# Kernel optimization log

Hardware: AMD Instinct MI355X
Metric: run time of the kernel (lower is better)

The kernel has to match this reference:

```python
import jax, jax.numpy as jnp
import numpy as np

PATCH = 32      # patch_size
OUT = 224       # output_size
K = 9           # num_patches (3x3 grid)
GRID = 3


def _srm_kernel():
    # filter1 + filter2 + filter3 combined (as in SRMConv._get_srm_kernels)
    f = np.array([[-1., 3., -1.], [3., -8., 3.], [-1., 3., -1.]], dtype=np.float32)
    k = np.zeros((3, 3, 3, 3), dtype=np.float32)
    for i in range(3):
        k[i, i] = f
    return jnp.asarray(k)


def setup_inputs() -> dict:
    key = jax.random.key(0)
    x = jax.random.uniform(key, (16, 3, 1024, 1024), dtype=jnp.float32)
    return {"x": x, "srm_kernel": _srm_kernel()}


def reference(x, srm_kernel):
    B, C, H, W = x.shape
    nh, nw = H // PATCH, W // PATCH
    # [N, B, C, P, P], N patches in row-major (i, j) order to match the loop
    p = x.reshape(B, C, nh, PATCH, nw, PATCH).transpose(2, 4, 0, 1, 3, 5)
    p = p.reshape(nh * nw, B, C, PATCH, PATCH)

    dx = jnp.abs(p[..., 1:] - p[..., :-1])
    dy = jnp.abs(p[..., 1:, :] - p[..., :-1, :])
    ax = (1, 2, 3, 4)  # stats over the whole batch, as in the original .item() scoring
    grad_mean = (dx.mean(axis=ax) + dy.mean(axis=ax)) * 0.5
    grad_var = (jnp.var(dx, axis=ax, ddof=1) + jnp.var(dy, axis=ax, ddof=1)) * 0.5
    score = grad_mean * grad_var                      # [N]

    order = jnp.argsort(score)                        # ascending, like np.argsort
    rich = p[order[-K:]]                              # [9, B, C, P, P]
    poor = p[order[:K]]

    def reconstruct(ps):
        # 3x3 grid of PATCH x PATCH patches -> [B, C, 3P, 3P]
        g = ps.reshape(GRID, GRID, B, C, PATCH, PATCH)
        return g.transpose(2, 3, 0, 4, 1, 5).reshape(B, C, GRID * PATCH, GRID * PATCH)

    def upsample(img):
        # bilinear, align_corners=False (half-pixel centers), upsampling so antialias is a no-op
        return jax.image.resize(img, (B, C, OUT, OUT), method='bilinear')

    def srm(img):
        return jax.lax.conv_general_dilated(
            img, srm_kernel, window_strides=(1, 1), padding=((1, 1), (1, 1)),
            dimension_numbers=('NCHW', 'OIHW', 'NCHW'))

    rich_srm = srm(upsample(reconstruct(rich)))       # [B, 3, 224, 224]
    poor_srm = srm(upsample(reconstruct(poor)))
    return jnp.stack([rich_srm, poor_srm])            # [2, B, 3, 224, 224]
```

## Files before the change

### kernel.cpp

```cpp
#include <hip/hip_runtime.h>


#define NSLICE 48
#define IMG    1048576

__global__ __launch_bounds__(256) void k_score(const float* __restrict__ x,
                                               double* __restrict__ part) {
  const int ph = blockIdx.x;
  const int s  = blockIdx.y;
  const int t  = threadIdx.x;
  const float* base = x + (size_t)s * IMG + (size_t)ph * 32768 + 4 * t;

  double s1x = 0.0, s2x = 0.0, s1y = 0.0, s2y = 0.0;
  const bool has_d3 = (t & 7) != 7;

#define LD(r) (*(const float4*)(base + (size_t)(r) * 1024))
#define DX(v) { float nx = __shfl_down((v).x, 1);                              \
    float d0 = fabsf((v).y-(v).x), d1 = fabsf((v).z-(v).y),                    \
          d2 = fabsf((v).w-(v).z);                                             \
    float d3 = has_d3 ? fabsf(nx-(v).w) : 0.f;                                 \
    s1x += (double)((d0+d1)+(d2+d3));                                          \
    s2x += (double)((d0*d0+d1*d1)+(d2*d2+d3*d3)); }
#define DY(a,b) { float e0 = fabsf((b).x-(a).x), e1 = fabsf((b).y-(a).y),      \
                        e2 = fabsf((b).z-(a).z), e3 = fabsf((b).w-(a).w);      \
    s1y += (double)((e0+e1)+(e2+e3));                                          \
    s2y += (double)((e0*e0+e1*e1)+(e2*e2+e3*e3)); }

  float4 v0 = LD(0);
  for (int r = 0; r < 32; r += 8) {
    float4 w1 = LD(r + 1), w2 = LD(r + 2), w3 = LD(r + 3), w4 = LD(r + 4);
    float4 w5 = LD(r + 5), w6 = LD(r + 6), w7 = LD(r + 7);
    float4 w8;
    const bool more = (r + 8 < 32);
    if (more) w8 = LD(r + 8);
    DX(v0); DX(w1); DX(w2); DX(w3); DX(w4); DX(w5); DX(w6); DX(w7);
    DY(v0, w1); DY(w1, w2); DY(w2, w3); DY(w3, w4);
    DY(w4, w5); DY(w5, w6); DY(w6, w7);
    if (more) { DY(w7, w8); v0 = w8; }
  }
#undef LD
#undef DX
#undef DY

#pragma unroll
  for (int off = 4; off > 0; off >>= 1) {
    s1x += __shfl_down(s1x, off, 8);
    s2x += __shfl_down(s2x, off, 8);
    s1y += __shfl_down(s1y, off, 8);
    s2y += __shfl_down(s2y, off, 8);
  }
  if ((t & 7) == 0) {
    const int p = ph * 32 + (t >> 3);
    part[(size_t)(0 * NSLICE + s) * 1024 + p] = s1x;
    part[(size_t)(1 * NSLICE + s) * 1024 + p] = s2x;
    part[(size_t)(2 * NSLICE + s) * 1024 + p] = s1y;
    part[(size_t)(3 * NSLICE + s) * 1024 + p] = s2y;
  }
}

__global__ __launch_bounds__(256) void k_finalize(const double* __restrict__ part,
                                                  double* __restrict__ scores) {
  const int p    = blockIdx.x;
  const int t    = threadIdx.x;
  const int q    = t >> 6;
  const int lane = t & 63;

  double v = 0.0;
  if (lane < NSLICE)
    v = part[(size_t)(q * NSLICE + lane) * 1024 + p];

#pragma unroll
  for (int off = 32; off > 0; off >>= 1) v += __shfl_down(v, off);

  __shared__ double S[4];
  if (lane == 0) S[q] = v;
  __syncthreads();

  if (t == 0) {
    const double N = 47616.0;
    double mx = S[0] / N, my = S[2] / N;
    double vx = (S[1] - S[0] * S[0] / N) / (N - 1.0);
    double vy = (S[3] - S[2] * S[2] / N) / (N - 1.0);
    scores[p] = 0.25 * (mx + my) * (vx + vy);
  }
}

__global__ __launch_bounds__(256) void k_rank(const double* __restrict__ scores,
                                              int* __restrict__ sel) {
  __shared__ double sc[1024];
  const int t = threadIdx.x;
  for (int i = t; i < 1024; i += 256) sc[i] = scores[i];
  __syncthreads();

  const int c = blockIdx.x * 32 + (t >> 3);
  const double mine = sc[c];
  int rank = 0;
  for (int j = (t & 7); j < 1024; j += 8) {
    double vj = sc[j];
    rank += (vj < mine) || (vj == mine && j < c);
  }
#pragma unroll
  for (int off = 4; off > 0; off >>= 1) rank += __shfl_down(rank, off, 8);
  if ((t & 7) == 0) {
    if (rank < 9)          sel[9 + rank]    = c;
    else if (rank >= 1015) sel[rank - 1015] = c;
  }
}

__global__ __launch_bounds__(256) void k_output(const float* __restrict__ x,
                                                const int* __restrict__ sel,
                                                float* __restrict__ out) {
  const int gb   = blockIdx.x;
  const int blk  = gb / 56;
  const int y0   = (gb % 56) * 4;
  const int t    = threadIdx.x;
  const int w    = t >> 6;
  const int lane = t & 63;
  const int y    = y0 + w;

  const int set = blk / 48;
  const int bc  = blk % 48;

  __shared__ float S[4][3][96];

  int   ay[3], by[3];
  float fy[3];
  bool  vy[3];
  int s0;
  {
    const int Ylo  = max(y - 1, 0);
    int numl = 3 * Ylo - 2;
    s0 = numl < 0 ? 0 : min(numl / 7, 95);
#pragma unroll
    for (int q = 0; q < 3; ++q) {
      int Y  = y - 1 + q;
      vy[q]  = ((unsigned)Y < 224u);
      int Yc = min(max(Y, 0), 223);
      int num = 3 * Yc - 2;
      int i0  = num < 0 ? 0 : num / 7;
      float fr = num < 0 ? 0.f : (float)(num - 7 * i0) * (1.f / 7.f);
      if (i0 >= 95) { i0 = 95; fr = 0.f; }
      ay[q] = i0 - s0;
      by[q] = min(i0 + 1, 95) - s0;
      fy[q] = fr;
    }
  }

  const float* src = x + (size_t)bc * IMG;
  for (int ii = lane; ii < 72; ii += 64) {
    int r    = ii / 24;
    int c4   = (ii % 24) * 4;
    int srow = min(s0 + r, 95);
    int gr = srow >> 5, si = srow & 31;
    int gc = c4 >> 5,   j  = c4 & 31;
    int pidx = sel[set * 9 + gr * 3 + gc];
    const float4 v = *(const float4*)&src[(size_t)((pidx >> 5) * 32 + si) * 1024
                                          + (pidx & 31) * 32 + j];
    *(float4*)&S[w][r][c4] = v;
  }
  __syncthreads();

  float A[4], M[4];
#pragma unroll
  for (int k = 0; k < 4; ++k) {
    int xx = lane + (k << 6);
    int xc = min(xx, 223);
    int num = 3 * xc - 2;
    int ix0 = num < 0 ? 0 : num / 7;
    float fx = num < 0 ? 0.f : (float)(num - 7 * ix0) * (1.f / 7.f);
    if (ix0 >= 95) { ix0 = 95; fx = 0.f; }
    int ix1 = min(ix0 + 1, 95);

    float h0a = S[w][0][ix0], h0b = S[w][0][ix1];
    float h1a = S[w][1][ix0], h1b = S[w][1][ix1];
    float h2a = S[w][2][ix0], h2b = S[w][2][ix1];
    float h0 = h0a + fx * (h0b - h0a);
    float h1 = h1a + fx * (h1b - h1a);
    float h2 = h2a + fx * (h2b - h2a);

    float U3[3];
#pragma unroll
    for (int q = 0; q < 3; ++q) {
      float ha = (ay[q] == 0) ? h0 : h1;
      float hb = (by[q] == 0) ? h0 : ((by[q] == 1) ? h1 : h2);
      U3[q] = vy[q] ? (ha + fy[q] * (hb - ha)) : 0.f;
    }
    A[k] = U3[0] + U3[2];
    M[k] = U3[1];
  }

  float* o = out + (size_t)blk * (224 * 224) + (size_t)y * 224;
#pragma unroll
  for (int k = 0; k < 4; ++k) {
    int xx = lane + (k << 6);

    float aL = __shfl_up(A[k], 1);
    float mL = __shfl_up(M[k], 1);
    float aP = (k > 0) ? __shfl(A[k - 1], 63) : 0.f;
    float mP = (k > 0) ? __shfl(M[k - 1], 63) : 0.f;
    if (lane == 0) { aL = aP; mL = mP; }

    float aR = __shfl_down(A[k], 1);
    float mR = __shfl_down(M[k], 1);
    float aN = (k < 3) ? __shfl(A[k + 1], 0) : 0.f;
    float mN = (k < 3) ? __shfl(M[k + 1], 0) : 0.f;
    if (lane == 63) { aR = aN; mR = mN; }

    if (xx == 0)   { aL = 0.f; mL = 0.f; }
    if (xx == 223) { aR = 0.f; mR = 0.f; }

    if (xx < 224)
      o[xx] = 3.f * (A[k] + mL + mR) - (aL + aR) - 8.f * M[k];
  }
}

extern "C" void kernel_launch(void* const* d_in, const int* in_sizes, int n_in,
                              void* d_out, int out_size, void* d_ws, size_t ws_size,
                              hipStream_t stream) {
  const float* x = (const float*)d_in[0];
  float* out = (float*)d_out;

  double* part   = (double*)d_ws;
  double* scores = (double*)((char*)d_ws + 1572864);
  int*    sel    = (int*)((char*)d_ws + 1581056);

  k_score   <<<dim3(32, 48), 256, 0, stream>>>(x, part);
  k_finalize<<<1024, 256, 0, stream>>>(part, scores);
  k_rank    <<<32, 256, 0, stream>>>(scores, sel);
  k_output  <<<5376, 256, 0, stream>>>(x, sel, out);
}
```

Before: 64.39 us.

## Fuse finalize and rank via last-block atomic ticket; vectorize output stores

Merges the score-finalize and ranking kernels into one launch: each block finalizes one patch score, takes an atomic ticket, and the last block ranks all 1024 scores with one thread per patch. This removes a kernel launch and its gap. The ticket counter is reset inside the score kernel. The output kernel now gives each lane 4 consecutive columns, so neighbours come from registers and each row is written with float4 stores. In exchange, the finrank blocks are 1024 threads wide with mostly idle threads, and the ranking runs as a serial 1024-step loop in a single block.

```diff
diff --git a/kernel.cpp b/kernel.cpp
--- a/kernel.cpp
+++ b/kernel.cpp
@@ -5,10 +5,13 @@
 #define IMG    1048576
 
 __global__ __launch_bounds__(256) void k_score(const float* __restrict__ x,
-                                               double* __restrict__ part) {
+                                               double* __restrict__ part,
+                                               unsigned* __restrict__ counter) {
   const int ph = blockIdx.x;
   const int s  = blockIdx.y;
   const int t  = threadIdx.x;
+  if (ph == 0 && s == 0 && t == 0) *counter = 0u;
+
   const float* base = x + (size_t)s * IMG + (size_t)ph * 32768 + 4 * t;
 
   double s1x = 0.0, s2x = 0.0, s1y = 0.0, s2y = 0.0;
@@ -58,53 +61,53 @@
   }
 }
 
-__global__ __launch_bounds__(256) void k_finalize(const double* __restrict__ part,
-                                                  double* __restrict__ scores) {
-  const int p    = blockIdx.x;
-  const int t    = threadIdx.x;
-  const int q    = t >> 6;
-  const int lane = t & 63;
-
-  double v = 0.0;
-  if (lane < NSLICE)
-    v = part[(size_t)(q * NSLICE + lane) * 1024 + p];
-
-#pragma unroll
-  for (int off = 32; off > 0; off >>= 1) v += __shfl_down(v, off);
-
-  __shared__ double S[4];
-  if (lane == 0) S[q] = v;
+__global__ __launch_bounds__(1024) void k_finrank(const double* __restrict__ part,
+                                                  double* __restrict__ scores,
+                                                  int* __restrict__ sel,
+                                                  unsigned* __restrict__ counter) {
+  const int p = blockIdx.x;
+  const int t = threadIdx.x;
+  __shared__ double S4[4];
+  __shared__ int lastflag;
+
+  if (t < 256) {
+    const int q    = t >> 6;
+    const int lane = t & 63;
+    double v = 0.0;
+    if (lane < NSLICE)
+      v = part[(size_t)(q * NSLICE + lane) * 1024 + p];
+#pragma unroll
+    for (int off = 32; off > 0; off >>= 1) v += __shfl_down(v, off);
+    if (lane == 0) S4[q] = v;
+  }
   __syncthreads();
 
   if (t == 0) {
     const double N = 47616.0;
-    double mx = S[0] / N, my = S[2] / N;
-    double vx = (S[1] - S[0] * S[0] / N) / (N - 1.0);
-    double vy = (S[3] - S[2] * S[2] / N) / (N - 1.0);
+    double mx = S4[0] / N, my = S4[2] / N;
+    double vx = (S4[1] - S4[0] * S4[0] / N) / (N - 1.0);
+    double vy = (S4[3] - S4[2] * S4[2] / N) / (N - 1.0);
     scores[p] = 0.25 * (mx + my) * (vx + vy);
-  }
-}
-
-__global__ __launch_bounds__(256) void k_rank(const double* __restrict__ scores,
-                                              int* __restrict__ sel) {
+    __threadfence();
+    unsigned ticket = atomicAdd(counter, 1u);
+    lastflag = (ticket == 1023u) ? 1 : 0;
+  }
+  __syncthreads();
+  if (!lastflag) return;
+
+  __threadfence();
   __shared__ double sc[1024];
-  const int t = threadIdx.x;
-  for (int i = t; i < 1024; i += 256) sc[i] = scores[i];
-  __syncthreads();
-
-  const int c = blockIdx.x * 32 + (t >> 3);
-  const double mine = sc[c];
+  const double mine = scores[t];
+  sc[t] = mine;
+  __syncthreads();
+
   int rank = 0;
-  for (int j = (t & 7); j < 1024; j += 8) {
+  for (int j = 0; j < 1024; ++j) {
     double vj = sc[j];
-    rank += (vj < mine) || (vj == mine && j < c);
-  }
-#pragma unroll
-  for (int off = 4; off > 0; off >>= 1) rank += __shfl_down(rank, off, 8);
-  if ((t & 7) == 0) {
-    if (rank < 9)          sel[9 + rank]    = c;
-    else if (rank >= 1015) sel[rank - 1015] = c;
-  }
+    rank += (vj < mine) || (vj == mine && j < t);
+  }
+  if (rank < 9)          sel[9 + rank]    = t;
+  else if (rank >= 1015) sel[rank - 1015] = t;
 }
 
 __global__ __launch_bounds__(256) void k_output(const float* __restrict__ x,
@@ -160,10 +163,11 @@
   }
   __syncthreads();
 
+  const int xs = lane << 2;
   float A[4], M[4];
 #pragma unroll
   for (int k = 0; k < 4; ++k) {
-    int xx = lane + (k << 6);
+    int xx = xs + k;
     int xc = min(xx, 223);
     int num = 3 * xc - 2;
     int ix0 = num < 0 ? 0 : num / 7;
@@ -189,28 +193,26 @@
     M[k] = U3[1];
   }
 
-  float* o = out + (size_t)blk * (224 * 224) + (size_t)y * 224;
+  float aLs = __shfl_up(A[3], 1),  mLs = __shfl_up(M[3], 1);
+  float aRs = __shfl_down(A[0], 1), mRs = __shfl_down(M[0], 1);
+
+  float4 res;
+  float* rp = &res.x;
 #pragma unroll
   for (int k = 0; k < 4; ++k) {
-    int xx = lane + (k << 6);
-
-    float aL = __shfl_up(A[k], 1);
-    float mL = __shfl_up(M[k], 1);
-    float aP = (k > 0) ? __shfl(A[k - 1], 63) : 0.f;
-    float mP = (k > 0) ? __shfl(M[k - 1], 63) : 0.f;
-    if (lane == 0) { aL = aP; mL = mP; }
-
-    float aR = __shfl_down(A[k], 1);
-    float mR = __shfl_down(M[k], 1);
-    float aN = (k < 3) ? __shfl(A[k + 1], 0) : 0.f;
-    float mN = (k < 3) ? __shfl(M[k + 1], 0) : 0.f;
-    if (lane == 63) { aR = aN; mR = mN; }
-
+    int xx = xs + k;
+    float aL = (k > 0) ? A[k - 1] : aLs;
+    float mL = (k > 0) ? M[k - 1] : mLs;
+    float aR = (k < 3) ? A[k + 1] : aRs;
+    float mR = (k < 3) ? M[k + 1] : mRs;
     if (xx == 0)   { aL = 0.f; mL = 0.f; }
     if (xx == 223) { aR = 0.f; mR = 0.f; }
-
-    if (xx < 224)
-      o[xx] = 3.f * (A[k] + mL + mR) - (aL + aR) - 8.f * M[k];
+    rp[k] = 3.f * (A[k] + mL + mR) - (aL + aR) - 8.f * M[k];
+  }
+
+  if (lane < 56) {
+    float* o = out + (size_t)blk * (224 * 224) + (size_t)y * 224;
+    *(float4*)&o[xs] = res;
   }
 }
 
@@ -220,12 +222,12 @@
   const float* x = (const float*)d_in[0];
   float* out = (float*)d_out;
 
-  double* part   = (double*)d_ws;
-  double* scores = (double*)((char*)d_ws + 1572864);
-  int*    sel    = (int*)((char*)d_ws + 1581056);
-
-  k_score   <<<dim3(32, 48), 256, 0, stream>>>(x, part);
-  k_finalize<<<1024, 256, 0, stream>>>(part, scores);
-  k_rank    <<<32, 256, 0, stream>>>(scores, sel);
-  k_output  <<<5376, 256, 0, stream>>>(x, sel, out);
-}
+  double*   part    = (double*)d_ws;
+  double*   scores  = (double*)((char*)d_ws + 1572864);
+  int*      sel     = (int*)((char*)d_ws + 1581056);
+  unsigned* counter = (unsigned*)((char*)d_ws + 1581184);
+
+  k_score  <<<dim3(32, 48), 256, 0, stream>>>(x, part, counter);
+  k_finrank<<<1024, 1024, 0, stream>>>(part, scores, sel, counter);
+  k_output <<<5376, 256, 0, stream>>>(x, sel, out);
+}
```

Result: slower. 118.5 us (+84.0%).
